# Performance work log

Hardware: AMD Instinct MI355X
Metric: run time of the kernel (lower is better)

## Reference

```python
import jax, jax.numpy as jnp
import numpy as np

L, C, F, K = 8192, 2048, 128, 257  # timesteps, input_size, filter_size, lag (odd => symmetric 'same' pad)
NY = 256  # number of overwritten channel rows


def setup_inputs() -> dict:
    key = jax.random.key(0)
    k1, k2, k3, k4 = jax.random.split(key, 4)
    x = jax.random.normal(k1, (L, C), dtype=jnp.float32)
    Yt = jax.random.randint(k2, (NY,), 0, C)
    # learned parameters (torch.rand -> uniform[0,1))
    g = jax.random.uniform(k3, (C, F), dtype=jnp.float32)
    kernel = jax.random.uniform(k4, (F, K), dtype=jnp.float32)
    return {"x": x, "Yt": Yt, "g": g, "kernel": kernel}


def reference(x, Yt, g, kernel):
    # synapse[c] is the per-channel 1D filter; the original builds a dense
    # (C, C, K) kernel whose only non-zero slices are the diagonal, so the
    # full conv1d is mathematically a depthwise (grouped) conv.
    synapse = jnp.matmul(g, kernel)          # (C, K)
    lhs = x.T[None]                          # (1, C, L)  NCH
    rhs = synapse[:, None, :]                # (C, 1, K)  OIH, groups=C
    pad = (kernel.shape[1] - 1) // 2         # torch padding='same', odd K
    out = jax.lax.conv_general_dilated(
        lhs, rhs,
        window_strides=(1,),
        padding=[(pad, pad)],
        feature_group_count=x.shape[1],
        dimension_numbers=("NCH", "OIH", "NCH"),
    )                                        # (1, C, L)
    # result[:, Yt, :] = x.T[Yt] : scatter-overwrite selected channel rows
    out = out.at[:, Yt, :].set(x.T[Yt][None])
    return out
```

## Files before the change

### kernel.cpp

```cpp
#include <hip/hip_runtime.h>

#define LL   8192
#define CC   2048
#define FF   128
#define KK   257
#define PAD  128

#define SROWP 328
#define NT   18
#define NCH  8
#define NW   4
#define ROWS 1288

typedef __bf16 bf16x8 __attribute__((ext_vector_type(8)));
typedef float  f32x16 __attribute__((ext_vector_type(16)));

static __device__ __forceinline__ unsigned short f2bf(float f) {
    unsigned u = __float_as_uint(f);
    u = (u + 0x7fffu + ((u >> 16) & 1u)) >> 16;
    return (unsigned short)u;
}

__global__ __launch_bounds__(256) void synb_kernel(const float* __restrict__ g,
                                                   const float* __restrict__ kern,
                                                   const int* __restrict__ Yt, int ny,
                                                   unsigned short* __restrict__ synEb) {
    __shared__ int sfl[4];
    const int c0 = blockIdx.x * 4;
    const int t  = threadIdx.x;
    if (t < 4) sfl[t] = 0;
    __syncthreads();
    for (int i = t; i < ny; i += 256) {
        int y = Yt[i];
        #pragma unroll
        for (int ii = 0; ii < 4; ++ii) if (y == c0 + ii) sfl[ii] = 1;
    }
    __syncthreads();
    const float* g0 = g + (size_t)(c0 + 0) * FF;
    const float* g1 = g + (size_t)(c0 + 1) * FF;
    const float* g2 = g + (size_t)(c0 + 2) * FF;
    const float* g3 = g + (size_t)(c0 + 3) * FF;
    const int fl0 = sfl[0], fl1 = sfl[1], fl2 = sfl[2], fl3 = sfl[3];
    for (int p = t; p < SROWP; p += 256) {
        const int kk = p - 32;
        float a0 = 0.f, a1 = 0.f, a2 = 0.f, a3 = 0.f;
        const bool inr = (kk >= 0) && (kk < KK);
        if (inr) {
            #pragma unroll 8
            for (int f = 0; f < FF; ++f) {
                float kv = kern[f * KK + kk];
                a0 += kv * g0[f];
                a1 += kv * g1[f];
                a2 += kv * g2[f];
                a3 += kv * g3[f];
            }
        }
        float dlt = (kk == PAD) ? 1.f : 0.f;
        float v0 = inr ? (fl0 ? dlt : a0) : 0.f;
        float v1 = inr ? (fl1 ? dlt : a1) : 0.f;
        float v2 = inr ? (fl2 ? dlt : a2) : 0.f;
        float v3 = inr ? (fl3 ? dlt : a3) : 0.f;
        synEb[(size_t)(c0 + 0) * SROWP + p] = f2bf(v0);
        synEb[(size_t)(c0 + 1) * SROWP + p] = f2bf(v1);
        synEb[(size_t)(c0 + 2) * SROWP + p] = f2bf(v2);
        synEb[(size_t)(c0 + 3) * SROWP + p] = f2bf(v3);
    }
}

static __device__ __forceinline__ void stage_issue(const float* __restrict__ x,
                                                   int W0, int c0, int t,
                                                   float4* ev, float4* ov) {
    #pragma unroll
    for (int k = 0; k < 5; ++k) {
        int pidx = (k << 8) + t;
        int ch4  = pidx & 1;
        int pp   = pidx >> 1;
        int lg   = W0 + (pp << 1) - 128;
        const float* sp = x + (size_t)lg * CC + c0 + (ch4 << 2);
        float4 a = make_float4(0.f, 0.f, 0.f, 0.f);
        float4 b = make_float4(0.f, 0.f, 0.f, 0.f);
        if ((unsigned)lg       < (unsigned)LL) a = *(const float4*)sp;
        if ((unsigned)(lg + 1) < (unsigned)LL) b = *(const float4*)(sp + CC);
        ev[k] = a; ov[k] = b;
    }
}

static __device__ __forceinline__ void stage_write(unsigned short (*buf)[ROWS], int t,
                                                   const float4* ev, const float4* ov) {
    #pragma unroll
    for (int k = 0; k < 5; ++k) {
        int pidx = (k << 8) + t;
        int ch4  = pidx & 1;
        int pp   = pidx >> 1;
        int gq   = pp >> 2;
        int gp   = gq ^ ((gq >> 3) & 7);
        int dw   = (gp << 2) | (pp & 3);
        const float* pe = (const float*)&ev[k];
        const float* po = (const float*)&ov[k];
        #pragma unroll
        for (int c2 = 0; c2 < 4; ++c2) {
            unsigned val = (unsigned)f2bf(pe[c2]) | ((unsigned)f2bf(po[c2]) << 16);
            ((unsigned*)buf[(ch4 << 2) + c2])[dw] = val;
        }
    }
}

__global__ __launch_bounds__(256, 2) void fused_conv(const float* __restrict__ x,
                                                     const unsigned short* __restrict__ synEb,
                                                     float* __restrict__ out) {
    __shared__ alignas(16) unsigned short xch[2][NCH][ROWS];
    __shared__ alignas(16) unsigned short synL[NCH][SROWP];
    const int t = threadIdx.x;

    const int d    = (blockIdx.y << 1) | blockIdx.x;
    const int grp  = ((d >> 6) << 3) | (d & 7);
    const int rnk  = (d >> 3) & 7;
    const int cg   = (grp << 2) | (rnk >> 1);
    const int bx   = rnk & 1;
    const int c0 = cg << 3;
    const int L0 = bx << 12;

    {
        const int rr = t >> 5, u0 = t & 31;
        const unsigned* src = (const unsigned*)(synEb + (size_t)(c0 + rr) * SROWP);
        unsigned* dst = (unsigned*)synL[rr];
        for (int u = u0; u < SROWP / 2; u += 32) dst[u] = src[u];
    }

    const int w_id = t >> 6, ln = t & 63;
    const int j = ln & 31, q = ln >> 5;
    const int bb  = (q << 4) - 2 * j + 64;
    const int dwb = bb >> 2;
    const int sh  = (bb & 2) << 3;
    const int gb  = (j << 2) + q;

    float4 ev[5], ov[5];
    stage_issue(x, L0, c0, t, ev, ov);
    stage_write(xch[0], t, ev, ov);
    __syncthreads();

    for (int w = 0; w < NW; ++w) {
        const int cur = w & 1;
        const int W0  = L0 + (w << 10);
        if (w + 1 < NW) stage_issue(x, W0 + 1024, c0, t, ev, ov);

        #pragma unroll
        for (int cc = 0; cc < 2; ++cc) {
            const int ci = (w_id << 1) + cc;
            const unsigned* rp = (const unsigned*)(synL[ci]) + dwb;
            f32x16 acc;
            #pragma unroll
            for (int r = 0; r < 16; ++r) acc[r] = 0.f;
            #pragma unroll
            for (int m = 0; m < NT; ++m) {
                unsigned w0 = rp[(m << 3) + 0], w1 = rp[(m << 3) + 1], w2 = rp[(m << 3) + 2],
                         w3 = rp[(m << 3) + 3], w4 = rp[(m << 3) + 4];
                union { unsigned dd[4]; bf16x8 v; } B;
                B.dd[0] = (unsigned)((((unsigned long long)w1 << 32) | w0) >> sh);
                B.dd[1] = (unsigned)((((unsigned long long)w2 << 32) | w1) >> sh);
                B.dd[2] = (unsigned)((((unsigned long long)w3 << 32) | w2) >> sh);
                B.dd[3] = (unsigned)((((unsigned long long)w4 << 32) | w3) >> sh);
                int gq2 = gb + (m << 1);
                int gp2 = gq2 ^ ((gq2 >> 3) & 7);
                union { int4 i4; bf16x8 v; } A;
                A.i4 = *(const int4*)(&xch[cur][ci][gp2 << 3]);
                acc = __builtin_amdgcn_mfma_f32_32x32x16_bf16(A.v, B.v, acc, 0, 0, 0);
            }
            float* o = out + (size_t)(c0 + ci) * LL + W0 + j;
            #pragma unroll
            for (int r = 0; r < 16; ++r) {
                int row = (r & 3) + ((r >> 2) << 3) + (q << 2);
                o[row << 5] = acc[r];
            }
        }
        __syncthreads();
        if (w + 1 < NW) stage_write(xch[cur ^ 1], t, ev, ov);
        __syncthreads();
    }
}

extern "C" void kernel_launch(void* const* d_in, const int* in_sizes, int n_in,
                              void* d_out, int out_size, void* d_ws, size_t ws_size,
                              hipStream_t stream) {
    const float* x    = (const float*)d_in[0];
    const int*   Yt   = (const int*)  d_in[1];
    const float* g    = (const float*)d_in[2];
    const float* kern = (const float*)d_in[3];
    float* out = (float*)d_out;
    const int ny = in_sizes[1];

    unsigned short* synEb = (unsigned short*)d_ws;

    synb_kernel<<<CC / 4, 256, 0, stream>>>(g, kern, Yt, ny, synEb);
    fused_conv<<<dim3(2, 256), 256, 0, stream>>>(x, synEb, out);
}
```

Measured before the change: 157.4 us.

## Use one 512-thread block per channel group with register-resident filter fragments

Each block now covers the full 8192-step timeline for its 8 channels, running 8 windows instead of 4, with 512 threads so each wave owns one channel. The per-channel Toeplitz B fragments are built once and kept in registers, and the A-operand LDS offsets are precomputed, which takes the repeated shifted LDS reads and swizzle arithmetic out of the inner loop. Staging loads use float2 across more threads, and synL is filled once per block rather than twice. The trade-offs are half as many blocks (256) for the GPU's compute units, higher register pressure from 18 held fragments, and a longer serial window loop per block.

New measurement: 155.3 us. About the same (-1.3%).

```diff
diff --git a/kernel.cpp b/kernel.cpp
--- a/kernel.cpp
+++ b/kernel.cpp
@@ -9,7 +9,7 @@
 #define SROWP 328
 #define NT   18
 #define NCH  8
-#define NW   4
+#define NW   8
 #define ROWS 1288
 
 typedef __bf16 bf16x8 __attribute__((ext_vector_type(8)));
@@ -69,109 +69,118 @@
 
 static __device__ __forceinline__ void stage_issue(const float* __restrict__ x,
                                                    int W0, int c0, int t,
-                                                   float4* ev, float4* ov) {
+                                                   float2* ev, float2* ov) {
     #pragma unroll
     for (int k = 0; k < 5; ++k) {
-        int pidx = (k << 8) + t;
-        int ch4  = pidx & 1;
-        int pp   = pidx >> 1;
+        int pidx = (k << 9) + t;
+        int ch2  = pidx & 3;
+        int pp   = pidx >> 2;
         int lg   = W0 + (pp << 1) - 128;
-        const float* sp = x + (size_t)lg * CC + c0 + (ch4 << 2);
-        float4 a = make_float4(0.f, 0.f, 0.f, 0.f);
-        float4 b = make_float4(0.f, 0.f, 0.f, 0.f);
-        if ((unsigned)lg       < (unsigned)LL) a = *(const float4*)sp;
-        if ((unsigned)(lg + 1) < (unsigned)LL) b = *(const float4*)(sp + CC);
+        const float* sp = x + (size_t)lg * CC + c0 + (ch2 << 1);
+        float2 a = make_float2(0.f, 0.f);
+        float2 b = make_float2(0.f, 0.f);
+        if ((unsigned)lg       < (unsigned)LL) a = *(const float2*)sp;
+        if ((unsigned)(lg + 1) < (unsigned)LL) b = *(const float2*)(sp + CC);
         ev[k] = a; ov[k] = b;
     }
 }
 
 static __device__ __forceinline__ void stage_write(unsigned short (*buf)[ROWS], int t,
-                                                   const float4* ev, const float4* ov) {
+                                                   const float2* ev, const float2* ov) {
     #pragma unroll
     for (int k = 0; k < 5; ++k) {
-        int pidx = (k << 8) + t;
-        int ch4  = pidx & 1;
-        int pp   = pidx >> 1;
+        int pidx = (k << 9) + t;
+        int ch2  = pidx & 3;
+        int pp   = pidx >> 2;
         int gq   = pp >> 2;
         int gp   = gq ^ ((gq >> 3) & 7);
         int dw   = (gp << 2) | (pp & 3);
         const float* pe = (const float*)&ev[k];
         const float* po = (const float*)&ov[k];
         #pragma unroll
-        for (int c2 = 0; c2 < 4; ++c2) {
+        for (int c2 = 0; c2 < 2; ++c2) {
             unsigned val = (unsigned)f2bf(pe[c2]) | ((unsigned)f2bf(po[c2]) << 16);
-            ((unsigned*)buf[(ch4 << 2) + c2])[dw] = val;
-        }
-    }
-}
-
-__global__ __launch_bounds__(256, 2) void fused_conv(const float* __restrict__ x,
+            ((unsigned*)buf[(ch2 << 1) + c2])[dw] = val;
+        }
+    }
+}
+
+__global__ __launch_bounds__(512, 2) void fused_conv(const float* __restrict__ x,
                                                      const unsigned short* __restrict__ synEb,
                                                      float* __restrict__ out) {
     __shared__ alignas(16) unsigned short xch[2][NCH][ROWS];
     __shared__ alignas(16) unsigned short synL[NCH][SROWP];
     const int t = threadIdx.x;
 
-    const int d    = (blockIdx.y << 1) | blockIdx.x;
-    const int grp  = ((d >> 6) << 3) | (d & 7);
-    const int rnk  = (d >> 3) & 7;
-    const int cg   = (grp << 2) | (rnk >> 1);
-    const int bx   = rnk & 1;
+    const int d  = blockIdx.x;
+    const int cg = ((d & 7) << 5) | (d >> 3);
     const int c0 = cg << 3;
-    const int L0 = bx << 12;
-
-    {
-        const int rr = t >> 5, u0 = t & 31;
-        const unsigned* src = (const unsigned*)(synEb + (size_t)(c0 + rr) * SROWP);
-        unsigned* dst = (unsigned*)synL[rr];
-        for (int u = u0; u < SROWP / 2; u += 32) dst[u] = src[u];
-    }
-
-    const int w_id = t >> 6, ln = t & 63;
+
+    const int ci = t >> 6;
+    const int ln = t & 63;
     const int j = ln & 31, q = ln >> 5;
     const int bb  = (q << 4) - 2 * j + 64;
     const int dwb = bb >> 2;
     const int sh  = (bb & 2) << 3;
     const int gb  = (j << 2) + q;
 
-    float4 ev[5], ov[5];
-    stage_issue(x, L0, c0, t, ev, ov);
+    float2 ev[5], ov[5];
+    stage_issue(x, 0, c0, t, ev, ov);
+
+    for (int u = t; u < NCH * (SROWP / 2); u += 512) {
+        int rr = u / (SROWP / 2), uu = u - rr * (SROWP / 2);
+        ((unsigned*)synL[rr])[uu] =
+            ((const unsigned*)(synEb + (size_t)(c0 + rr) * SROWP))[uu];
+    }
+    __syncthreads();
+
+    bf16x8 bfrag[NT];
+    {
+        const unsigned* rp = (const unsigned*)(synL[ci]) + dwb;
+        #pragma unroll
+        for (int m = 0; m < NT; ++m) {
+            unsigned w0 = rp[(m << 3) + 0], w1 = rp[(m << 3) + 1], w2 = rp[(m << 3) + 2],
+                     w3 = rp[(m << 3) + 3], w4 = rp[(m << 3) + 4];
+            union { unsigned dd[4]; bf16x8 v; } B;
+            B.dd[0] = (unsigned)((((unsigned long long)w1 << 32) | w0) >> sh);
+            B.dd[1] = (unsigned)((((unsigned long long)w2 << 32) | w1) >> sh);
+            B.dd[2] = (unsigned)((((unsigned long long)w3 << 32) | w2) >> sh);
+            B.dd[3] = (unsigned)((((unsigned long long)w4 << 32) | w3) >> sh);
+            bfrag[m] = B.v;
+        }
+    }
+
+    int aoff[NT];
+    #pragma unroll
+    for (int m = 0; m < NT; ++m) {
+        int gq2 = gb + (m << 1);
+        int gp2 = gq2 ^ ((gq2 >> 3) & 7);
+        aoff[m] = gp2 << 4;
+    }
+
     stage_write(xch[0], t, ev, ov);
     __syncthreads();
 
     for (int w = 0; w < NW; ++w) {
         const int cur = w & 1;
-        const int W0  = L0 + (w << 10);
+        const int W0  = w << 10;
         if (w + 1 < NW) stage_issue(x, W0 + 1024, c0, t, ev, ov);
 
-        #pragma unroll
-        for (int cc = 0; cc < 2; ++cc) {
-            const int ci = (w_id << 1) + cc;
-            const unsigned* rp = (const unsigned*)(synL[ci]) + dwb;
-            f32x16 acc;
-            #pragma unroll
-            for (int r = 0; r < 16; ++r) acc[r] = 0.f;
-            #pragma unroll
-            for (int m = 0; m < NT; ++m) {
-                unsigned w0 = rp[(m << 3) + 0], w1 = rp[(m << 3) + 1], w2 = rp[(m << 3) + 2],
-                         w3 = rp[(m << 3) + 3], w4 = rp[(m << 3) + 4];
-                union { unsigned dd[4]; bf16x8 v; } B;
-                B.dd[0] = (unsigned)((((unsigned long long)w1 << 32) | w0) >> sh);
-                B.dd[1] = (unsigned)((((unsigned long long)w2 << 32) | w1) >> sh);
-                B.dd[2] = (unsigned)((((unsigned long long)w3 << 32) | w2) >> sh);
-                B.dd[3] = (unsigned)((((unsigned long long)w4 << 32) | w3) >> sh);
-                int gq2 = gb + (m << 1);
-                int gp2 = gq2 ^ ((gq2 >> 3) & 7);
-                union { int4 i4; bf16x8 v; } A;
-                A.i4 = *(const int4*)(&xch[cur][ci][gp2 << 3]);
-                acc = __builtin_amdgcn_mfma_f32_32x32x16_bf16(A.v, B.v, acc, 0, 0, 0);
-            }
-            float* o = out + (size_t)(c0 + ci) * LL + W0 + j;
-            #pragma unroll
-            for (int r = 0; r < 16; ++r) {
-                int row = (r & 3) + ((r >> 2) << 3) + (q << 2);
-                o[row << 5] = acc[r];
-            }
+        const char* xrow = (const char*)xch[cur][ci];
+        f32x16 acc;
+        #pragma unroll
+        for (int r = 0; r < 16; ++r) acc[r] = 0.f;
+        #pragma unroll
+        for (int m = 0; m < NT; ++m) {
+            union { int4 i4; bf16x8 v; } A;
+            A.i4 = *(const int4*)(xrow + aoff[m]);
+            acc = __builtin_amdgcn_mfma_f32_32x32x16_bf16(A.v, bfrag[m], acc, 0, 0, 0);
+        }
+        float* o = out + (size_t)(c0 + ci) * LL + W0 + j;
+        #pragma unroll
+        for (int r = 0; r < 16; ++r) {
+            int row = (r & 3) + ((r >> 2) << 3) + (q << 2);
+            o[row << 5] = acc[r];
         }
         __syncthreads();
         if (w + 1 < NW) stage_write(xch[cur ^ 1], t, ev, ov);
@@ -192,5 +201,5 @@
     unsigned short* synEb = (unsigned short*)d_ws;
 
     synb_kernel<<<CC / 4, 256, 0, stream>>>(g, kern, Yt, ny, synEb);
-    fused_conv<<<dim3(2, 256), 256, 0, stream>>>(x, synEb, out);
-}
+    fused_conv<<<256, 512, 0, stream>>>(x, synEb, out);
+}
```
